# Kernel tuning notes

Hardware: AMD Instinct MI355X
Metric: run time of the kernel (lower is better)

## Reference

```python
import jax, jax.numpy as jnp
import numpy as np

N_CENTER = 4000
N_NEIGH = 16
N_FEAT = 64
N_ATOMS = 20000
N_SPECIES = 8
COS_EPS = 1e-8  # torch cosine_similarity eps


def setup_inputs() -> dict:
    key = jax.random.key(0)
    k1, k2, k3, k4, k5, k6 = jax.random.split(key, 6)
    atom_i_idx = jax.random.randint(k1, (N_CENTER,), 0, N_ATOMS, dtype=jnp.int32)
    atom_j_idx = jax.random.randint(k2, (N_CENTER, N_NEIGH), 0, N_ATOMS, dtype=jnp.int32)
    # physical distances in [0.5, 4.5) Angstrom to avoid near-zero divisions
    dist_ij = jax.random.uniform(k3, (N_CENTER, N_NEIGH), dtype=jnp.float32) * 4.0 + 0.5
    atoms_xyz = jax.random.normal(k4, (N_ATOMS, 3), dtype=jnp.float32) * 5.0
    atoms_long = jax.random.randint(k5, (N_ATOMS, 2), 0, N_SPECIES, dtype=jnp.int32)
    embed_table = jax.random.normal(k6, (N_SPECIES, N_FEAT), dtype=jnp.float32)
    return {
        "nNeigh": N_NEIGH,
        "atom_i_idx": atom_i_idx,
        "atom_j_idx": atom_j_idx,
        "dist_ij": dist_ij,
        "atoms_xyz": atoms_xyz,
        "atoms_long": atoms_long,
        "embed_table": embed_table,
    }


def reference(nNeigh, atom_i_idx, atom_j_idx, dist_ij, atoms_xyz, atoms_long, embed_table):
    C = atom_i_idx.shape[0]
    N = nNeigh
    F = embed_table.shape[1]

    # --- triple geometry ---
    xyz_i = atoms_xyz[atom_i_idx][:, None, None, :]          # [C,1,1,3]
    xyz_j = atoms_xyz[atom_j_idx]                            # [C,N,3]
    vec_ij = xyz_j[:, :, None, :] - xyz_i                    # [C,N,1,3]
    vec_ik = xyz_j[:, None, :, :] - xyz_i                    # [C,1,N,3]

    dot = jnp.sum(vec_ij * vec_ik, axis=-1)                  # [C,N,N]
    norm_j = jnp.linalg.norm(vec_ij, axis=-1)                # [C,N,1]
    norm_k = jnp.linalg.norm(vec_ik, axis=-1)                # [C,1,N]
    cos = dot / (jnp.maximum(norm_j, COS_EPS) * jnp.maximum(norm_k, COS_EPS))
    ang = jnp.arccos(cos * 0.9999)                           # [C,N,N]

    d_ij = dist_ij[:, :, None, None]                         # [C,N,1,1]
    d_ik = dist_ij[:, None, :, None]                         # [C,1,N,1]

    # --- embeddings ---
    emb_i = embed_table[atoms_long[atom_i_idx, 1]]           # [C,F]
    emb_j = embed_table[atoms_long[atom_j_idx, 1]]           # [C,N,F]

    shp1 = (C, N, N, 1)
    shpF = (C, N, N, F)
    ang_desc = jnp.concatenate(
        (
            jnp.broadcast_to(d_ij, shp1),
            jnp.broadcast_to(d_ik, shp1),
            ang[..., None],
            jnp.broadcast_to(emb_i[:, None, None, :], shpF),
            jnp.broadcast_to(emb_j[:, :, None, :] / d_ij, shpF),
            jnp.broadcast_to(emb_j[:, None, :, :] / d_ik, shpF),
        ),
        axis=-1,
    )                                                         # [C,N,N,3+3F]

    # off-diagonal (j != k) triples, static index set
    jj, kk = np.nonzero(~np.eye(N, dtype=bool))
    ang_desc = ang_desc[:, jj, kk, :]                         # [C,N*(N-1),3+3F]
    return atom_i_idx.reshape(-1), ang_desc
```

## Files before the change

### kernel.cpp

```cpp
#include <hip/hip_runtime.h>
#include <math.h>

#define NNEI   16
#define NFEAT  64
#define NPAIR  240
#define ROWW   195
#define PER_C  (NPAIR * ROWW)
#define COS_EPS 1e-8f

typedef float f32x4 __attribute__((ext_vector_type(4)));

__device__ __forceinline__ int swz(int w) { return w ^ ((w >> 5) & 3); }

__device__ __forceinline__ int off_of(int p, int s) {
    const unsigned ju = (unsigned)p / 15u;
    const int j = (int)ju;
    const int r = p - (int)ju * 15;
    const int k = r + (r >= j);
    int off;
    if      (s >= 131) off = 336 + (k << 6) + (s - 131);
    else if (s >= 67)  off = 336 + (j << 6) + (s - 67);
    else if (s >= 3)   off = 269 + s;
    else if (s == 2)   off = (j << 4) + k;
    else if (s == 1)   off = 256 + k;
    else               off = 256 + j;
    return swz(off);
}

__global__ __launch_bounds__(256) void angdesc_kernel(
    const int*   __restrict__ atom_i_idx,
    const int*   __restrict__ atom_j_idx,
    const float* __restrict__ dist_ij,
    const float* __restrict__ atoms_xyz,
    const int*   __restrict__ atoms_long,
    const float* __restrict__ embed_table,
    float*       __restrict__ out0,
    float*       __restrict__ out1)
{
    __shared__ float s_lds[1360];
    __shared__ float s_vec[NNEI][3];
    __shared__ float s_nrm[NNEI];
    __shared__ float s_invd[NNEI];
    __shared__ int   s_spec[NNEI];

    const int c   = blockIdx.x;
    const int tid = threadIdx.x;
    const int ii  = atom_i_idx[c];

    if (tid == 0) out0[c] = (float)ii;

    const float xi = atoms_xyz[ii * 3 + 0];
    const float yi = atoms_xyz[ii * 3 + 1];
    const float zi = atoms_xyz[ii * 3 + 2];

    if (tid < NNEI) {
        const int jn = atom_j_idx[c * NNEI + tid];
        const float vx = atoms_xyz[jn * 3 + 0] - xi;
        const float vy = atoms_xyz[jn * 3 + 1] - yi;
        const float vz = atoms_xyz[jn * 3 + 2] - zi;
        s_vec[tid][0] = vx; s_vec[tid][1] = vy; s_vec[tid][2] = vz;
        s_nrm[tid]  = sqrtf(vx * vx + vy * vy + vz * vz);
        const float d = dist_ij[c * NNEI + tid];
        s_lds[swz(256 + tid)] = d;
        s_invd[tid] = 1.0f / d;
        s_spec[tid] = atoms_long[jn * 2 + 1];
    } else if (tid >= 64 && tid < 128) {
        const int f = tid - 64;
        const int speci = atoms_long[ii * 2 + 1];
        s_lds[swz(272 + f)] = embed_table[speci * NFEAT + f];
    }
    __syncthreads();

    {
        const int j = tid >> 4, k = tid & 15;
        const float dot = s_vec[j][0] * s_vec[k][0]
                        + s_vec[j][1] * s_vec[k][1]
                        + s_vec[j][2] * s_vec[k][2];
        const float nj = fmaxf(s_nrm[j], COS_EPS);
        const float nk = fmaxf(s_nrm[k], COS_EPS);
        const float cosv = dot / (nj * nk);
        s_lds[swz(tid)] = acosf(cosv * 0.9999f);
    }
    for (int e = tid; e < NNEI * NFEAT; e += 256) {
        const int n = e >> 6, f = e & 63;
        s_lds[swz(336 + e)] = embed_table[s_spec[n] * NFEAT + f] * s_invd[n];
    }
    __syncthreads();

    f32x4* __restrict__ dst4 = (f32x4*)(out1 + (size_t)c * PER_C);

    int p = (tid << 2) / 195;
    int s = (tid << 2) - p * 195;
    #pragma unroll 2
    for (int q = tid; q < PER_C / 4; q += 256) {
        f32x4 v;
        #pragma unroll
        for (int i = 0; i < 4; ++i) {
            int pp = p, ss = s + i;
            if (ss >= 195) { pp += 1; ss -= 195; }
            v[i] = s_lds[off_of(pp, ss)];
        }
        __builtin_nontemporal_store(v, dst4 + q);
        s += 49; p += 5;
        if (s >= 195) { s -= 195; p += 1; }
    }
}

extern "C" void kernel_launch(void* const* d_in, const int* in_sizes, int n_in,
                              void* d_out, int out_size, void* d_ws, size_t ws_size,
                              hipStream_t stream) {
    const int*   atom_i_idx  = (const int*)  d_in[1];
    const int*   atom_j_idx  = (const int*)  d_in[2];
    const float* dist_ij     = (const float*)d_in[3];
    const float* atoms_xyz   = (const float*)d_in[4];
    const int*   atoms_long  = (const int*)  d_in[5];
    const float* embed_table = (const float*)d_in[6];

    const int C = in_sizes[1];
    float* out  = (float*)d_out;
    (void)d_ws; (void)ws_size;

    angdesc_kernel<<<C, 256, 0, stream>>>(atom_i_idx, atom_j_idx, dist_ij,
                                          atoms_xyz, atoms_long, embed_table,
                                          out, out + C);
}
```

Before: 770.1 us.

## Split kernel into image-build and expand passes via workspace buffer

Splits the fused kernel in two when workspace is large enough. The first kernel computes each center's compact LDS image (angles, distances, scaled embeddings) and writes it to global workspace. The second reloads that image into LDS and streams the expanded descriptor rows to the output. The aim is to separate the latency-bound gather and acos phase from the bandwidth-bound store phase, so the store kernel runs at full occupancy without stalls. This costs an extra launch and a global write and read of the image, and falls back to the fused kernel otherwise.

Result: no change. 783.1 us (+1.7%).

```diff
diff --git a/kernel.cpp b/kernel.cpp
--- a/kernel.cpp
+++ b/kernel.cpp
@@ -6,6 +6,8 @@
 #define NPAIR  240
 #define ROWW   195
 #define PER_C  (NPAIR * ROWW)
+#define IMG    1360
+#define IMG4   (IMG / 4)
 #define COS_EPS 1e-8f
 
 typedef float f32x4 __attribute__((ext_vector_type(4)));
@@ -27,27 +29,19 @@
     return swz(off);
 }
 
-__global__ __launch_bounds__(256) void angdesc_kernel(
+__device__ __forceinline__ void build_image(
+    int c, int tid,
     const int*   __restrict__ atom_i_idx,
     const int*   __restrict__ atom_j_idx,
     const float* __restrict__ dist_ij,
     const float* __restrict__ atoms_xyz,
     const int*   __restrict__ atoms_long,
     const float* __restrict__ embed_table,
-    float*       __restrict__ out0,
-    float*       __restrict__ out1)
-{
-    __shared__ float s_lds[1360];
-    __shared__ float s_vec[NNEI][3];
-    __shared__ float s_nrm[NNEI];
-    __shared__ float s_invd[NNEI];
-    __shared__ int   s_spec[NNEI];
-
-    const int c   = blockIdx.x;
-    const int tid = threadIdx.x;
-    const int ii  = atom_i_idx[c];
-
-    if (tid == 0) out0[c] = (float)ii;
+    float* __restrict__ s_lds,
+    float (* __restrict__ s_vec)[3], float* __restrict__ s_nrm,
+    float* __restrict__ s_invd, int* __restrict__ s_spec)
+{
+    const int ii = atom_i_idx[c];
 
     const float xi = atoms_xyz[ii * 3 + 0];
     const float yi = atoms_xyz[ii * 3 + 1];
@@ -86,9 +80,12 @@
         s_lds[swz(336 + e)] = embed_table[s_spec[n] * NFEAT + f] * s_invd[n];
     }
     __syncthreads();
-
+}
+
+__device__ __forceinline__ void expand_from_lds(
+    int c, int tid, const float* __restrict__ s_lds, float* __restrict__ out1)
+{
     f32x4* __restrict__ dst4 = (f32x4*)(out1 + (size_t)c * PER_C);
-
     int p = (tid << 2) / 195;
     int s = (tid << 2) - p * 195;
     #pragma unroll 2
@@ -106,6 +103,75 @@
     }
 }
 
+__global__ __launch_bounds__(256) void img_build(
+    const int*   __restrict__ atom_i_idx,
+    const int*   __restrict__ atom_j_idx,
+    const float* __restrict__ dist_ij,
+    const float* __restrict__ atoms_xyz,
+    const int*   __restrict__ atoms_long,
+    const float* __restrict__ embed_table,
+    float*       __restrict__ img,
+    float*       __restrict__ out0)
+{
+    alignas(16) __shared__ float s_lds[IMG];
+    __shared__ float s_vec[NNEI][3];
+    __shared__ float s_nrm[NNEI];
+    __shared__ float s_invd[NNEI];
+    __shared__ int   s_spec[NNEI];
+
+    const int c   = blockIdx.x;
+    const int tid = threadIdx.x;
+    if (tid == 0) out0[c] = (float)atom_i_idx[c];
+
+    build_image(c, tid, atom_i_idx, atom_j_idx, dist_ij, atoms_xyz,
+                atoms_long, embed_table, s_lds, s_vec, s_nrm, s_invd, s_spec);
+
+    f32x4* __restrict__ dst = (f32x4*)(img + (size_t)c * IMG);
+    const f32x4* __restrict__ src = (const f32x4*)s_lds;
+    for (int t = tid; t < IMG4; t += 256) dst[t] = src[t];
+}
+
+__global__ __launch_bounds__(256) void img_expand(
+    const float* __restrict__ img,
+    float*       __restrict__ out1)
+{
+    alignas(16) __shared__ float s_lds[IMG];
+    const int c   = blockIdx.x;
+    const int tid = threadIdx.x;
+
+    const f32x4* __restrict__ src = (const f32x4*)(img + (size_t)c * IMG);
+    f32x4* __restrict__ s4 = (f32x4*)s_lds;
+    for (int t = tid; t < IMG4; t += 256) s4[t] = src[t];
+    __syncthreads();
+
+    expand_from_lds(c, tid, s_lds, out1);
+}
+
+__global__ __launch_bounds__(256) void angdesc_fused(
+    const int*   __restrict__ atom_i_idx,
+    const int*   __restrict__ atom_j_idx,
+    const float* __restrict__ dist_ij,
+    const float* __restrict__ atoms_xyz,
+    const int*   __restrict__ atoms_long,
+    const float* __restrict__ embed_table,
+    float*       __restrict__ out0,
+    float*       __restrict__ out1)
+{
+    alignas(16) __shared__ float s_lds[IMG];
+    __shared__ float s_vec[NNEI][3];
+    __shared__ float s_nrm[NNEI];
+    __shared__ float s_invd[NNEI];
+    __shared__ int   s_spec[NNEI];
+
+    const int c   = blockIdx.x;
+    const int tid = threadIdx.x;
+    if (tid == 0) out0[c] = (float)atom_i_idx[c];
+
+    build_image(c, tid, atom_i_idx, atom_j_idx, dist_ij, atoms_xyz,
+                atoms_long, embed_table, s_lds, s_vec, s_nrm, s_invd, s_spec);
+    expand_from_lds(c, tid, s_lds, out1);
+}
+
 extern "C" void kernel_launch(void* const* d_in, const int* in_sizes, int n_in,
                               void* d_out, int out_size, void* d_ws, size_t ws_size,
                               hipStream_t stream) {
@@ -118,9 +184,17 @@
 
     const int C = in_sizes[1];
     float* out  = (float*)d_out;
-    (void)d_ws; (void)ws_size;
-
-    angdesc_kernel<<<C, 256, 0, stream>>>(atom_i_idx, atom_j_idx, dist_ij,
-                                          atoms_xyz, atoms_long, embed_table,
-                                          out, out + C);
-}
+
+    const size_t need = (size_t)C * IMG * sizeof(float);
+    if (ws_size >= need && d_ws != nullptr) {
+        float* img = (float*)d_ws;
+        img_build<<<C, 256, 0, stream>>>(atom_i_idx, atom_j_idx, dist_ij,
+                                         atoms_xyz, atoms_long, embed_table,
+                                         img, out);
+        img_expand<<<C, 256, 0, stream>>>(img, out + C);
+    } else {
+        angdesc_fused<<<C, 256, 0, stream>>>(atom_i_idx, atom_j_idx, dist_ij,
+                                             atoms_xyz, atoms_long, embed_table,
+                                             out, out + C);
+    }
+}
```

## Write output rows per wavefront with scalar coalesced stores instead of vectorized gather

Applied to the files above, without the earlier changes.

Replaces the flat float4 store loop, which decoded pair and column indices per element, with a row-oriented scheme. Each wavefront owns one j and writes the 195-float rows for all k as four strided scalar stores per lane, with the first three lanes carrying the header scalars. This removes the per-element index arithmetic and division. In exchange it gives up 16-byte nontemporal stores for unaligned 4-byte stores, since 195-float rows are not 16-byte aligned.

Result: no change. 765.1 us (-0.7%).

```diff
diff --git a/kernel.cpp b/kernel.cpp
--- a/kernel.cpp
+++ b/kernel.cpp
@@ -6,26 +6,10 @@
 #define NPAIR  240
 #define ROWW   195
 #define PER_C  (NPAIR * ROWW)
+#define IMG    1360
 #define COS_EPS 1e-8f
 
-typedef float f32x4 __attribute__((ext_vector_type(4)));
-
 __device__ __forceinline__ int swz(int w) { return w ^ ((w >> 5) & 3); }
-
-__device__ __forceinline__ int off_of(int p, int s) {
-    const unsigned ju = (unsigned)p / 15u;
-    const int j = (int)ju;
-    const int r = p - (int)ju * 15;
-    const int k = r + (r >= j);
-    int off;
-    if      (s >= 131) off = 336 + (k << 6) + (s - 131);
-    else if (s >= 67)  off = 336 + (j << 6) + (s - 67);
-    else if (s >= 3)   off = 269 + s;
-    else if (s == 2)   off = (j << 4) + k;
-    else if (s == 1)   off = 256 + k;
-    else               off = 256 + j;
-    return swz(off);
-}
 
 __global__ __launch_bounds__(256) void angdesc_kernel(
     const int*   __restrict__ atom_i_idx,
@@ -37,7 +21,7 @@
     float*       __restrict__ out0,
     float*       __restrict__ out1)
 {
-    __shared__ float s_lds[1360];
+    __shared__ float s_lds[IMG];
     __shared__ float s_vec[NNEI][3];
     __shared__ float s_nrm[NNEI];
     __shared__ float s_invd[NNEI];
@@ -78,8 +62,7 @@
                         + s_vec[j][2] * s_vec[k][2];
         const float nj = fmaxf(s_nrm[j], COS_EPS);
         const float nk = fmaxf(s_nrm[k], COS_EPS);
-        const float cosv = dot / (nj * nk);
-        s_lds[swz(tid)] = acosf(cosv * 0.9999f);
+        s_lds[swz(tid)] = acosf((dot / (nj * nk)) * 0.9999f);
     }
     for (int e = tid; e < NNEI * NFEAT; e += 256) {
         const int n = e >> 6, f = e & 63;
@@ -87,22 +70,36 @@
     }
     __syncthreads();
 
-    f32x4* __restrict__ dst4 = (f32x4*)(out1 + (size_t)c * PER_C);
+    const int l  = tid & 63;
+    const int w  = tid >> 6;
+    const int sh = (l - 3) & 63;
+    const bool head = (l < 3);
 
-    int p = (tid << 2) / 195;
-    int s = (tid << 2) - p * 195;
-    #pragma unroll 2
-    for (int q = tid; q < PER_C / 4; q += 256) {
-        f32x4 v;
+    const float Ri = s_lds[swz(272 + sh)];
+
+    for (int jj = 0; jj < 4; ++jj) {
+        const int j = (jj << 2) | w;
+        const float Rj = s_lds[swz(336 + (j << 6) + sh)];
+        const float v2 = head ? Ri : Rj;
+
         #pragma unroll
-        for (int i = 0; i < 4; ++i) {
-            int pp = p, ss = s + i;
-            if (ss >= 195) { pp += 1; ss -= 195; }
-            v[i] = s_lds[off_of(pp, ss)];
+        for (int k = 0; k < 16; ++k) {
+            if (k == j) continue;
+            const float Rk = s_lds[swz(336 + (k << 6) + sh)];
+            const int sa = (l == 1) ? swz(256 + k)
+                         : (l == 2) ? swz((j << 4) + k)
+                                    : swz(256 + j);
+            const float sc = s_lds[sa];
+            const float v1 = head ? sc : Ri;
+            const float v3 = head ? Rj : Rk;
+
+            const int p = j * 15 + k - (k > j);
+            float* __restrict__ rp = out1 + (size_t)c * PER_C + (size_t)p * ROWW;
+            rp[l]        = v1;
+            rp[l + 64]   = v2;
+            rp[l + 128]  = v3;
+            if (head) rp[l + 192] = Rk;
         }
-        __builtin_nontemporal_store(v, dst4 + q);
-        s += 49; p += 5;
-        if (s >= 195) { s -= 195; p += 1; }
     }
 }
 
```
